# Optimization experiments

Hardware: AMD Instinct MI355X
Metric: run time of the kernel (lower is better)

The kernel has to match this reference:

```python
import jax, jax.numpy as jnp
import numpy as np

N = 50000      # nodes (src = dst at both layers)
E = 800000     # edges per layer
T = 8          # time steps
C_IN = 16      # input channels
HID = 16       # conv1 out channels (hardcoded in SAGENet)
C_OUT = 32     # final out channels


def setup_inputs() -> dict:
    key = jax.random.key(0)
    ks = jax.random.split(key, 10)
    X = jax.random.normal(ks[0], (T, N, C_IN), dtype=jnp.float32)
    edge_index0 = jax.random.randint(ks[1], (2, E), 0, N, dtype=jnp.int32)
    edge_weight0 = jax.random.uniform(ks[2], (E,), dtype=jnp.float32)
    edge_index1 = jax.random.randint(ks[3], (2, E), 0, N, dtype=jnp.int32)
    edge_weight1 = jax.random.uniform(ks[4], (E,), dtype=jnp.float32)
    res_n_id0 = jnp.arange(N, dtype=jnp.int32)
    res_n_id1 = jnp.arange(N, dtype=jnp.int32)
    W1 = jax.random.normal(ks[5], (2 * C_IN, HID), dtype=jnp.float32) * 0.1
    b1 = jax.random.normal(ks[6], (HID,), dtype=jnp.float32) * 0.1
    W2 = jax.random.normal(ks[7], (2 * HID, C_OUT), dtype=jnp.float32) * 0.1
    b2 = jax.random.normal(ks[8], (C_OUT,), dtype=jnp.float32) * 0.1
    return {"X": X, "edge_index0": edge_index0, "edge_weight0": edge_weight0,
            "edge_index1": edge_index1, "edge_weight1": edge_weight1,
            "res_n_id0": res_n_id0, "res_n_id1": res_n_id1,
            "W1": W1, "b1": b1, "W2": W2, "b2": b2}


def sage_conv(x, edge_index, edge_weight, res_n_id, num_dst, W, b):
    # x: [N_src, T, C]; message = edge_weight * x[src]; mean-aggregate to dst;
    # concat residual x[res_n_id] then linear (old PyG SAGEConv, concat=True).
    src, dst = edge_index[0], edge_index[1]
    msg = x[src] * edge_weight[:, None, None]                      # [E, T, C]
    summed = jax.ops.segment_sum(msg, dst, num_segments=num_dst)   # [Nd, T, C]
    cnt = jax.ops.segment_sum(jnp.ones_like(edge_weight), dst, num_segments=num_dst)
    aggr = summed / jnp.maximum(cnt, 1.0)[:, None, None]
    h = jnp.concatenate([x[res_n_id], aggr], axis=-1)              # [Nd, T, 2C]
    return jnp.einsum('ntc,cd->ntd', h, W) + b


def reference(X, edge_index0, edge_weight0, edge_index1, edge_weight1,
              res_n_id0, res_n_id1, W1, b1, W2, b2):
    x = jnp.transpose(X, (1, 0, 2))                                # [N, T, C]
    x = jax.nn.leaky_relu(sage_conv(x, edge_index0, edge_weight0, res_n_id0, N, W1, b1), 0.01)
    x = jax.nn.leaky_relu(sage_conv(x, edge_index1, edge_weight1, res_n_id1, N, W2, b2), 0.01)
    return jnp.transpose(x, (1, 0, 2))                             # [T, N, C_out]
```

## Files before the change

### kernel.cpp

```cpp
#include <hip/hip_runtime.h>
#include <hip/hip_bf16.h>
#include <stdint.h>

static constexpr int Nn   = 50000;
static constexpr int Ee   = 800000;
static constexpr int Tt   = 8;
static constexpr int CIN  = 16;
static constexpr int HID  = 16;
static constexpr int COUT = 32;
static constexpr int TC   = Tt * CIN;
static constexpr int ROWD = TC / 2;

static constexpr int NB  = (2 * Nn + 255) / 256;
static constexpr int CAP = 16;

static constexpr int WBUF_FLOATS = 1584;

__device__ inline float bflo(uint32_t u) { return __uint_as_float(u << 16); }
__device__ inline float bfhi(uint32_t u) { return __uint_as_float(u & 0xffff0000u); }
__device__ inline unsigned short f2bf(float x) {
    __hip_bfloat16 h = __float2bfloat16(x);
    unsigned short u; __builtin_memcpy(&u, &h, 2); return u;
}
__device__ inline uint32_t bfpack(float a, float b) {
    return (uint32_t)f2bf(a) | ((uint32_t)f2bf(b) << 16);
}

__global__ void k_detect_stage(const unsigned short* __restrict__ x16, int nvals,
                               int* __restrict__ flag,
                               const void* W1, const void* b1,
                               const void* W2, const void* b2,
                               float* __restrict__ wbuf,
                               int* __restrict__ bucketCnt) {
    __shared__ int bad;
    if (threadIdx.x == 0) bad = 0;
    __syncthreads();
    for (int i = threadIdx.x; i < nvals; i += 256) {
        int ex = (x16[i] >> 7) & 0xFF;
        if (ex >= 0x8D) atomicOr(&bad, 1);
    }
    __syncthreads();
    int f = bad;
    if (threadIdx.x == 0) flag[0] = f;
    for (int i = threadIdx.x; i < NB; i += 256) bucketCnt[i] = 0;
    for (int i = threadIdx.x; i < WBUF_FLOATS; i += 256) {
        const void* src; int idx;
        if (i < 512)       { src = W1; idx = i; }
        else if (i < 528)  { src = b1; idx = i - 512; }
        else if (i < 1552) { src = W2; idx = i - 528; }
        else               { src = b2; idx = i - 1552; }
        wbuf[i] = f ? ((const float*)src)[idx]
                    : __bfloat162float(((const __hip_bfloat16*)src)[idx]);
    }
}


__global__ __launch_bounds__(256) void k_count(const int* __restrict__ ei0,
                                               const int* __restrict__ ei1,
                                               int* __restrict__ bucketCnt) {
    __shared__ int hist[NB];
    for (int i = threadIdx.x; i < NB; i += 256) hist[i] = 0;
    __syncthreads();
    const int4* d0 = (const int4*)(ei0 + Ee);
    const int4* d1 = (const int4*)(ei1 + Ee);
    int stride = gridDim.x * 256;
    int nq = Ee / 4;
    for (int i = blockIdx.x * 256 + threadIdx.x; i < 2 * nq; i += stride) {
        int4 v; int addn;
        if (i < nq) { v = d0[i]; addn = 0; }
        else        { v = d1[i - nq]; addn = Nn; }
        atomicAdd(&hist[(v.x + addn) >> 8], 1);
        atomicAdd(&hist[(v.y + addn) >> 8], 1);
        atomicAdd(&hist[(v.z + addn) >> 8], 1);
        atomicAdd(&hist[(v.w + addn) >> 8], 1);
    }
    __syncthreads();
    for (int i = threadIdx.x; i < NB; i += 256)
        if (hist[i]) atomicAdd(&bucketCnt[i], hist[i]);
}

__global__ void k_bucketscan(const int* __restrict__ bucketCnt,
                             int* __restrict__ base, int* __restrict__ gcur) {
    __shared__ int tmp[512];
    int tid = threadIdx.x;
    int v = (tid < NB) ? bucketCnt[tid] : 0;
    tmp[tid] = v;
    __syncthreads();
    for (int ofs = 1; ofs < 512; ofs <<= 1) {
        int t = (tid >= ofs) ? tmp[tid - ofs] : 0;
        __syncthreads();
        tmp[tid] += t;
        __syncthreads();
    }
    if (tid < NB) { int b = tmp[tid] - v; base[tid] = b; gcur[tid] = b; }
    if (tid == 0) base[NB] = 2 * Ee;
}

__global__ __launch_bounds__(256) void k_bin(const int* __restrict__ flag,
        const int* __restrict__ ei0, const void* w0v,
        const int* __restrict__ ei1, const void* w1v,
        int* __restrict__ gcur, uint64_t* __restrict__ gout) {
    __shared__ uint64_t rows[NB][CAP];
    __shared__ int cnt[NB];
    int tid = threadIdx.x;
    for (int i = tid; i < NB; i += 256) cnt[i] = 0;
    __syncthreads();
    int f = flag[0];
    int tileStride = gridDim.x * 256;
    for (int base_e = blockIdx.x * 256; base_e < 2 * Ee; base_e += tileStride) {
        int e = base_e + tid;
        if (e < 2 * Ee) {
            int g; uint32_t src, wb;
            if (e < Ee) {
                g = ei0[Ee + e];
                src = (uint32_t)ei0[e];
                wb = f ? f2bf(((const float*)w0v)[e]) : ((const unsigned short*)w0v)[e];
            } else {
                int e1 = e - Ee;
                g = Nn + ei1[Ee + e1];
                src = (uint32_t)ei1[e1];
                wb = f ? f2bf(((const float*)w1v)[e1]) : ((const unsigned short*)w1v)[e1];
            }
            uint64_t r = ((uint64_t)(uint32_t)g << 32) | (src << 16) | wb;
            int b = g >> 8;
            int idx = atomicAdd(&cnt[b], 1);
            if (idx < CAP) rows[b][idx] = r;
            else { int pos = atomicAdd(&gcur[b], 1); gout[pos] = r; }
        }
        __syncthreads();
        for (int b = tid; b < NB; b += 256) {
            if (cnt[b] >= CAP) {
                int pos = atomicAdd(&gcur[b], CAP);
#pragma unroll
                for (int k = 0; k < CAP; k++) gout[pos + k] = rows[b][k];
                cnt[b] = 0;
            }
        }
        __syncthreads();
    }
    for (int b = tid; b < NB; b += 256) {
        int c = cnt[b];
        if (c > 0) {
            int pos = atomicAdd(&gcur[b], c);
            for (int k = 0; k < c; k++) gout[pos + k] = rows[b][k];
        }
    }
}

__global__ __launch_bounds__(256) void k_csr(const int* __restrict__ base,
        const uint64_t* __restrict__ gout,
        int* __restrict__ off, uint32_t* __restrict__ rec) {
    __shared__ int hist[256];
    __shared__ int tmp[256];
    __shared__ int cur[256];
    __shared__ uint32_t stage[8192];
    int b = blockIdx.x, tid = threadIdx.x;
    int lo = base[b], hi = base[b + 1];
    hist[tid] = 0;
    __syncthreads();
    for (int i = lo + tid; i < hi; i += 256) {
        int gl = (int)(gout[i] >> 32) & 255;
        atomicAdd(&hist[gl], 1);
    }
    __syncthreads();
    int v = hist[tid];
    tmp[tid] = v;
    __syncthreads();
    for (int ofs = 1; ofs < 256; ofs <<= 1) {
        int t = (tid >= ofs) ? tmp[tid - ofs] : 0;
        __syncthreads();
        tmp[tid] += t;
        __syncthreads();
    }
    int excl = tmp[tid] - v;
    int gg = (b << 8) + tid;
    if (gg < 2 * Nn) off[gg] = lo + excl;
    if (b == NB - 1 && tid == 0) off[2 * Nn] = 2 * Ee;
    int count = hi - lo;
    if (count <= 8192) {
        cur[tid] = excl;
        __syncthreads();
        for (int i = lo + tid; i < hi; i += 256) {
            uint64_t r = gout[i];
            int gl = (int)(r >> 32) & 255;
            int pos = atomicAdd(&cur[gl], 1);
            stage[pos] = (uint32_t)r;
        }
        __syncthreads();
        for (int i = tid; i < count; i += 256) rec[lo + i] = stage[i];
    } else {
        cur[tid] = lo + excl;
        __syncthreads();
        for (int i = lo + tid; i < hi; i += 256) {
            uint64_t r = gout[i];
            int gl = (int)(r >> 32) & 255;
            int pos = atomicAdd(&cur[gl], 1);
            rec[pos] = (uint32_t)r;
        }
    }
}

__global__ void k_transpose(const int* __restrict__ flag, const void* Xv,
                            uint32_t* __restrict__ xrows) {
    int f = flag[0];
    int i = blockIdx.x * blockDim.x + threadIdx.x;
    if (i >= Nn * ROWD) return;
    int n = i >> 6;
    int l = i & 63;
    int t = l >> 3;
    int c = (l & 7) * 2;
    int sidx = (t * Nn + n) * CIN + c;
    uint32_t v;
    if (f) {
        float2 ab = ((const float2*)Xv)[sidx >> 1];
        v = bfpack(ab.x, ab.y);
    } else {
        const unsigned short* u = (const unsigned short*)Xv;
        v = (uint32_t)u[sidx] | ((uint32_t)u[sidx + 1] << 16);
    }
    xrows[i] = v;
}


__global__ __launch_bounds__(256) void k_layer1(
    const uint32_t* __restrict__ xrows, const int* __restrict__ off,
    const uint32_t* __restrict__ rec, const int* __restrict__ resid,
    const float* __restrict__ wbuf, uint32_t* __restrict__ h1rows) {
    __shared__ float Ws[32 * 16];
    __shared__ float bs[16];
    __shared__ float sh[4][256];
    int tid = threadIdx.x;
    int wv = tid >> 6, lane = tid & 63;
    for (int i = tid; i < 512; i += 256) Ws[i] = wbuf[i];
    if (tid < 16) bs[tid] = wbuf[512 + tid];
    __syncthreads();
    int n = blockIdx.x * 4 + wv;
    int o0 = __builtin_amdgcn_readfirstlane(off[n]);
    int o1 = __builtin_amdgcn_readfirstlane(off[n + 1]);
    int rn = __builtin_amdgcn_readfirstlane(resid[n]);
    uint32_t xv = xrows[rn * ROWD + lane];
    float alo = 0.f, ahi = 0.f;
    int j = o0;
    for (; j + 8 <= o1; j += 8) {
        uint32_t e[8], g[8];
#pragma unroll
        for (int k = 0; k < 8; k++) e[k] = rec[j + k];
#pragma unroll
        for (int k = 0; k < 8; k++) g[k] = xrows[(e[k] >> 16) * ROWD + lane];
#pragma unroll
        for (int k = 0; k < 8; k++) {
            float w = bflo(e[k]);
            alo += w * bflo(g[k]);
            ahi += w * bfhi(g[k]);
        }
    }
    for (; j < o1; j++) {
        uint32_t e0 = rec[j];
        uint32_t g0 = xrows[(e0 >> 16) * ROWD + lane];
        float w0 = bflo(e0);
        alo += w0 * bflo(g0);
        ahi += w0 * bfhi(g0);
    }
    float inv = 1.f / (float)max(o1 - o0, 1);
    float* xs = &sh[wv][0];
    float* ag = &sh[wv][128];
    xs[2 * lane] = bflo(xv);
    xs[2 * lane + 1] = bfhi(xv);
    ag[2 * lane] = alo * inv;
    ag[2 * lane + 1] = ahi * inv;
    int t = lane >> 3;
    int c0 = (2 * lane) & 15;
    const float* xr = &xs[t * 16];
    const float* ar = &ag[t * 16];
    float v0 = bs[c0], v1 = bs[c0 + 1];
#pragma unroll
    for (int k = 0; k < 16; k++) {
        float xk = xr[k], ak = ar[k];
        v0 += xk * Ws[k * 16 + c0] + ak * Ws[(16 + k) * 16 + c0];
        v1 += xk * Ws[k * 16 + c0 + 1] + ak * Ws[(16 + k) * 16 + c0 + 1];
    }
    v0 = v0 > 0.f ? v0 : 0.01f * v0;
    v1 = v1 > 0.f ? v1 : 0.01f * v1;
    h1rows[n * ROWD + lane] = bfpack(v0, v1);
}

__global__ __launch_bounds__(256) void k_layer2(
    const int* __restrict__ flag,
    const uint32_t* __restrict__ h1rows, const int* __restrict__ off,
    const uint32_t* __restrict__ rec, const int* __restrict__ resid,
    const float* __restrict__ wbuf, void* __restrict__ outv) {
    __shared__ float Ws[32 * 32];
    __shared__ float bs[32];
    __shared__ float sh[4][256];
    int tid = threadIdx.x;
    int wv = tid >> 6, lane = tid & 63;
    for (int i = tid; i < 1024; i += 256) Ws[i] = wbuf[528 + i];
    if (tid < 32) bs[tid] = wbuf[1552 + tid];
    __syncthreads();
    int f = flag[0];
    int n = blockIdx.x * 4 + wv;
    int o0 = __builtin_amdgcn_readfirstlane(off[Nn + n]);
    int o1 = __builtin_amdgcn_readfirstlane(off[Nn + n + 1]);
    int rn = __builtin_amdgcn_readfirstlane(resid[n]);
    uint32_t xv = h1rows[rn * ROWD + lane];
    float alo = 0.f, ahi = 0.f;
    int j = o0;
    for (; j + 8 <= o1; j += 8) {
        uint32_t e[8], g[8];
#pragma unroll
        for (int k = 0; k < 8; k++) e[k] = rec[j + k];
#pragma unroll
        for (int k = 0; k < 8; k++) g[k] = h1rows[(e[k] >> 16) * ROWD + lane];
#pragma unroll
        for (int k = 0; k < 8; k++) {
            float w = bflo(e[k]);
            alo += w * bflo(g[k]);
            ahi += w * bfhi(g[k]);
        }
    }
    for (; j < o1; j++) {
        uint32_t e0 = rec[j];
        uint32_t g0 = h1rows[(e0 >> 16) * ROWD + lane];
        float w0 = bflo(e0);
        alo += w0 * bflo(g0);
        ahi += w0 * bfhi(g0);
    }
    float inv = 1.f / (float)max(o1 - o0, 1);
    float* xs = &sh[wv][0];
    float* ag = &sh[wv][128];
    xs[2 * lane] = bflo(xv);
    xs[2 * lane + 1] = bfhi(xv);
    ag[2 * lane] = alo * inv;
    ag[2 * lane + 1] = ahi * inv;
    int h = lane & 31;
    int tb = lane >> 5;
#pragma unroll
    for (int q = 0; q < 4; q++) {
        int t = tb + 2 * q;
        const float* xr = &xs[t * 16];
        const float* ar = &ag[t * 16];
        float v = bs[h];
#pragma unroll
        for (int k = 0; k < 16; k++) {
            v += xr[k] * Ws[k * 32 + h] + ar[k] * Ws[(16 + k) * 32 + h];
        }
        v = v > 0.f ? v : 0.01f * v;
        size_t idx = ((size_t)(t * Nn + n)) * COUT + h;
        if (f) ((float*)outv)[idx] = v;
        else   ((__hip_bfloat16*)outv)[idx] = __float2bfloat16(v);
    }
}


extern "C" void kernel_launch(void* const* d_in, const int* in_sizes, int n_in,
                              void* d_out, int out_size, void* d_ws, size_t ws_size,
                              hipStream_t stream) {
    const void* X   = d_in[0];
    const int* ei0  = (const int*)d_in[1];
    const void* w0  = d_in[2];
    const int* ei1  = (const int*)d_in[3];
    const void* w1  = d_in[4];
    const int* rn0  = (const int*)d_in[5];
    const int* rn1  = (const int*)d_in[6];
    const void* W1  = d_in[7];
    const void* b1  = d_in[8];
    const void* W2  = d_in[9];
    const void* b2  = d_in[10];

    char* ws = (char*)d_ws;
    size_t p = 0;
    auto alloc = [&](size_t bytes) -> char* {
        p = (p + 255) & ~(size_t)255;
        char* r = ws + p;
        p += bytes;
        return r;
    };
    int* flag       = (int*)alloc(4);
    float* wbuf     = (float*)alloc(WBUF_FLOATS * 4);
    int* bucketCnt  = (int*)alloc(NB * 4);
    int* base       = (int*)alloc((NB + 1) * 4);
    int* gcur       = (int*)alloc(NB * 4);
    int* off        = (int*)alloc(((size_t)2 * Nn + 1) * 4);
    uint32_t* recf  = (uint32_t*)alloc((size_t)2 * Ee * 4);
    uint32_t* h1rows= (uint32_t*)alloc((size_t)Nn * ROWD * 4);
    uint64_t* gout  = (uint64_t*)alloc((size_t)2 * Ee * 8);
    uint32_t* xrows = (uint32_t*)gout;

    hipLaunchKernelGGL(k_detect_stage, dim3(1), dim3(256), 0, stream,
                       (const unsigned short*)X, 16384, flag, W1, b1, W2, b2,
                       wbuf, bucketCnt);
    hipLaunchKernelGGL(k_count, dim3(256), dim3(256), 0, stream,
                       ei0, ei1, bucketCnt);
    hipLaunchKernelGGL(k_bucketscan, dim3(1), dim3(512), 0, stream,
                       bucketCnt, base, gcur);
    hipLaunchKernelGGL(k_bin, dim3(512), dim3(256), 0, stream,
                       flag, ei0, w0, ei1, w1, gcur, gout);
    hipLaunchKernelGGL(k_csr, dim3(NB), dim3(256), 0, stream,
                       base, gout, off, recf);
    hipLaunchKernelGGL(k_transpose, dim3((Nn * ROWD + 255) / 256), dim3(256), 0, stream,
                       flag, X, xrows);
    hipLaunchKernelGGL(k_layer1, dim3(Nn / 4), dim3(256), 0, stream,
                       xrows, off, recf, rn0, wbuf, h1rows);
    hipLaunchKernelGGL(k_layer2, dim3(Nn / 4), dim3(256), 0, stream,
                       flag, h1rows, off, recf, rn1, wbuf, d_out);
    (void)in_sizes; (void)n_in; (void)out_size; (void)ws_size;
}
```

Baseline: 276.3 us.

## Use MFMA for SAGE linear layers and 16-byte gathers with edge-parallel lanes

Both layer kernels now gather neighbor rows as 16-byte uint4 loads, with four lane groups each handling a different edge and a cross-lane shuffle reduction at the end. This replaces the per-lane 4-byte loads over edges. The dense concat-then-linear step now runs as bf16 MFMA 16x16x32 instructions on weights pre-packed by the setup kernel, instead of scalar FMAs reading float weights from shared memory. The binning kernel also processes four edges per thread per tile. The cost is that the aggregate and weights are rounded to bf16 before the matmul, which may change accuracy in fp32 mode.

```diff
diff --git a/kernel.cpp b/kernel.cpp
--- a/kernel.cpp
+++ b/kernel.cpp
@@ -14,7 +14,9 @@
 static constexpr int NB  = (2 * Nn + 255) / 256;
 static constexpr int CAP = 16;
 
-static constexpr int WBUF_FLOATS = 1584;
+typedef __attribute__((ext_vector_type(8))) short short8;
+typedef __attribute__((ext_vector_type(4))) float f32x4;
+union FU { uint4 u4; short8 s8; };
 
 __device__ inline float bflo(uint32_t u) { return __uint_as_float(u << 16); }
 __device__ inline float bfhi(uint32_t u) { return __uint_as_float(u & 0xffff0000u); }
@@ -25,33 +27,50 @@
 __device__ inline uint32_t bfpack(float a, float b) {
     return (uint32_t)f2bf(a) | ((uint32_t)f2bf(b) << 16);
 }
+__device__ inline void fma8(float2& a0, float2& a1, float2& a2, float2& a3,
+                            float w, uint4 r) {
+    a0.x += w * bflo(r.x); a0.y += w * bfhi(r.x);
+    a1.x += w * bflo(r.y); a1.y += w * bfhi(r.y);
+    a2.x += w * bflo(r.z); a2.y += w * bfhi(r.z);
+    a3.x += w * bflo(r.w); a3.y += w * bfhi(r.w);
+}
+__device__ inline void redg(float2& a) {
+    a.x += __shfl_xor(a.x, 16); a.y += __shfl_xor(a.y, 16);
+    a.x += __shfl_xor(a.x, 32); a.y += __shfl_xor(a.y, 32);
+}
 
 __global__ void k_detect_stage(const unsigned short* __restrict__ x16, int nvals,
                                int* __restrict__ flag,
                                const void* W1, const void* b1,
                                const void* W2, const void* b2,
-                               float* __restrict__ wbuf,
+                               float* __restrict__ biasbuf,
+                               uint32_t* __restrict__ wpk1,
+                               uint32_t* __restrict__ wpk2,
                                int* __restrict__ bucketCnt) {
     __shared__ int bad;
-    if (threadIdx.x == 0) bad = 0;
-    __syncthreads();
-    for (int i = threadIdx.x; i < nvals; i += 256) {
+    int tid = threadIdx.x;
+    if (tid == 0) bad = 0;
+    __syncthreads();
+    for (int i = tid; i < nvals; i += 256) {
         int ex = (x16[i] >> 7) & 0xFF;
         if (ex >= 0x8D) atomicOr(&bad, 1);
     }
     __syncthreads();
     int f = bad;
-    if (threadIdx.x == 0) flag[0] = f;
-    for (int i = threadIdx.x; i < NB; i += 256) bucketCnt[i] = 0;
-    for (int i = threadIdx.x; i < WBUF_FLOATS; i += 256) {
-        const void* src; int idx;
-        if (i < 512)       { src = W1; idx = i; }
-        else if (i < 528)  { src = b1; idx = i - 512; }
-        else if (i < 1552) { src = W2; idx = i - 528; }
-        else               { src = b2; idx = i - 1552; }
-        wbuf[i] = f ? ((const float*)src)[idx]
-                    : __bfloat162float(((const __hip_bfloat16*)src)[idx]);
-    }
+    if (tid == 0) flag[0] = f;
+    auto ldf = [&](const void* srcp, int idx) -> float {
+        return f ? ((const float*)srcp)[idx]
+                 : __bfloat162float(((const __hip_bfloat16*)srcp)[idx]);
+    };
+    if (tid < 16) biasbuf[tid] = ldf(b1, tid);
+    if (tid >= 16 && tid < 48) biasbuf[tid] = ldf(b2, tid - 16);
+    { int h = tid >> 4, d = tid & 15;
+      wpk1[tid] = bfpack(ldf(W1, 2 * d * 16 + h), ldf(W1, (2 * d + 1) * 16 + h)); }
+    for (int i = tid; i < 512; i += 256) {
+        int h = i >> 4, d = i & 15;
+        wpk2[i] = bfpack(ldf(W2, 2 * d * 32 + h), ldf(W2, (2 * d + 1) * 32 + h));
+    }
+    for (int i = tid; i < NB; i += 256) bucketCnt[i] = 0;
 }
 
 
@@ -106,26 +125,31 @@
     for (int i = tid; i < NB; i += 256) cnt[i] = 0;
     __syncthreads();
     int f = flag[0];
-    int tileStride = gridDim.x * 256;
-    for (int base_e = blockIdx.x * 256; base_e < 2 * Ee; base_e += tileStride) {
-        int e = base_e + tid;
-        if (e < 2 * Ee) {
-            int g; uint32_t src, wb;
-            if (e < Ee) {
-                g = ei0[Ee + e];
-                src = (uint32_t)ei0[e];
-                wb = f ? f2bf(((const float*)w0v)[e]) : ((const unsigned short*)w0v)[e];
-            } else {
-                int e1 = e - Ee;
-                g = Nn + ei1[Ee + e1];
-                src = (uint32_t)ei1[e1];
-                wb = f ? f2bf(((const float*)w1v)[e1]) : ((const unsigned short*)w1v)[e1];
+    int tileStride = gridDim.x * 1024;
+    for (int base_e = blockIdx.x * 1024; base_e < 2 * Ee; base_e += tileStride) {
+#pragma unroll
+        for (int s = 0; s < 4; s++) {
+            int e = base_e + s * 256 + tid;
+            if (e < 2 * Ee) {
+                int g; uint32_t src, wb;
+                if (e < Ee) {
+                    g = ei0[Ee + e];
+                    src = (uint32_t)ei0[e];
+                    wb = f ? f2bf(((const float*)w0v)[e])
+                           : ((const unsigned short*)w0v)[e];
+                } else {
+                    int e1 = e - Ee;
+                    g = Nn + ei1[Ee + e1];
+                    src = (uint32_t)ei1[e1];
+                    wb = f ? f2bf(((const float*)w1v)[e1])
+                           : ((const unsigned short*)w1v)[e1];
+                }
+                uint64_t r = ((uint64_t)(uint32_t)g << 32) | (src << 16) | wb;
+                int b = g >> 8;
+                int idx = atomicAdd(&cnt[b], 1);
+                if (idx < CAP) rows[b][idx] = r;
+                else { int pos = atomicAdd(&gcur[b], 1); gout[pos] = r; }
             }
-            uint64_t r = ((uint64_t)(uint32_t)g << 32) | (src << 16) | wb;
-            int b = g >> 8;
-            int idx = atomicAdd(&cnt[b], 1);
-            if (idx < CAP) rows[b][idx] = r;
-            else { int pos = atomicAdd(&gcur[b], 1); gout[pos] = r; }
         }
         __syncthreads();
         for (int b = tid; b < NB; b += 256) {
@@ -225,129 +249,126 @@
 __global__ __launch_bounds__(256) void k_layer1(
     const uint32_t* __restrict__ xrows, const int* __restrict__ off,
     const uint32_t* __restrict__ rec, const int* __restrict__ resid,
-    const float* __restrict__ wbuf, uint32_t* __restrict__ h1rows) {
-    __shared__ float Ws[32 * 16];
-    __shared__ float bs[16];
-    __shared__ float sh[4][256];
-    int tid = threadIdx.x;
-    int wv = tid >> 6, lane = tid & 63;
-    for (int i = tid; i < 512; i += 256) Ws[i] = wbuf[i];
-    if (tid < 16) bs[tid] = wbuf[512 + tid];
-    __syncthreads();
+    const uint32_t* __restrict__ wpk1, const float* __restrict__ biasbuf,
+    uint32_t* __restrict__ h1rows) {
+    __shared__ __align__(16) uint32_t shA[32 * 20];
+    int tid = threadIdx.x, wv = tid >> 6, lane = tid & 63;
+    int g = lane >> 4, p = lane & 15;
+    uint4 bfr = ((const uint4*)wpk1)[p * 4 + g];
+    float bias = biasbuf[p];
     int n = blockIdx.x * 4 + wv;
     int o0 = __builtin_amdgcn_readfirstlane(off[n]);
     int o1 = __builtin_amdgcn_readfirstlane(off[n + 1]);
     int rn = __builtin_amdgcn_readfirstlane(resid[n]);
-    uint32_t xv = xrows[rn * ROWD + lane];
-    float alo = 0.f, ahi = 0.f;
-    int j = o0;
-    for (; j + 8 <= o1; j += 8) {
-        uint32_t e[8], g[8];
+    const uint4* xb = (const uint4*)xrows;
+    uint4 xs4 = xb[rn * 16 + p];
+    float2 a0 = {0.f, 0.f}, a1 = a0, a2 = a0, a3 = a0;
+    for (int j = o0; j < o1; j += 8) {
+        int j0 = j + g, j1 = j + 4 + g;
+        uint32_t e0 = rec[min(j0, o1 - 1)];
+        uint32_t e1 = rec[min(j1, o1 - 1)];
+        uint4 r0 = xb[(int)(e0 >> 16) * 16 + p];
+        uint4 r1 = xb[(int)(e1 >> 16) * 16 + p];
+        float w0 = (j0 < o1) ? bflo(e0) : 0.f;
+        float w1 = (j1 < o1) ? bflo(e1) : 0.f;
+        fma8(a0, a1, a2, a3, w0, r0);
+        fma8(a0, a1, a2, a3, w1, r1);
+    }
+    redg(a0); redg(a1); redg(a2); redg(a3);
+    float inv = 1.f / (float)max(o1 - o0, 1);
+    uint4 agp;
+    agp.x = bfpack(a0.x * inv, a0.y * inv);
+    agp.y = bfpack(a1.x * inv, a1.y * inv);
+    agp.z = bfpack(a2.x * inv, a2.y * inv);
+    agp.w = bfpack(a3.x * inv, a3.y * inv);
+    int r = wv * 8 + (p >> 1);
+    int hs = (p & 1) * 4;
+    if (g == 0)      *(uint4*)&shA[r * 20 + hs] = xs4;
+    else if (g == 1) *(uint4*)&shA[r * 20 + 8 + hs] = agp;
+    __syncthreads();
+    FU fa, fb; fb.u4 = bfr;
+    fa.u4 = *(const uint4*)&shA[((wv >> 1) * 16 + p) * 20 + 4 * g];
+    f32x4 acc = {bias, bias, bias, bias};
+    acc = __builtin_amdgcn_mfma_f32_16x16x32_bf16(fa.s8, fb.s8, acc, 0, 0, 0);
+    bool mine = ((g >> 1) == (wv & 1));
 #pragma unroll
-        for (int k = 0; k < 8; k++) e[k] = rec[j + k];
-#pragma unroll
-        for (int k = 0; k < 8; k++) g[k] = xrows[(e[k] >> 16) * ROWD + lane];
-#pragma unroll
-        for (int k = 0; k < 8; k++) {
-            float w = bflo(e[k]);
-            alo += w * bflo(g[k]);
-            ahi += w * bfhi(g[k]);
-        }
-    }
-    for (; j < o1; j++) {
-        uint32_t e0 = rec[j];
-        uint32_t g0 = xrows[(e0 >> 16) * ROWD + lane];
-        float w0 = bflo(e0);
-        alo += w0 * bflo(g0);
-        ahi += w0 * bfhi(g0);
-    }
-    float inv = 1.f / (float)max(o1 - o0, 1);
-    float* xs = &sh[wv][0];
-    float* ag = &sh[wv][128];
-    xs[2 * lane] = bflo(xv);
-    xs[2 * lane + 1] = bfhi(xv);
-    ag[2 * lane] = alo * inv;
-    ag[2 * lane + 1] = ahi * inv;
-    int t = lane >> 3;
-    int c0 = (2 * lane) & 15;
-    const float* xr = &xs[t * 16];
-    const float* ar = &ag[t * 16];
-    float v0 = bs[c0], v1 = bs[c0 + 1];
-#pragma unroll
-    for (int k = 0; k < 16; k++) {
-        float xk = xr[k], ak = ar[k];
-        v0 += xk * Ws[k * 16 + c0] + ak * Ws[(16 + k) * 16 + c0];
-        v1 += xk * Ws[k * 16 + c0 + 1] + ak * Ws[(16 + k) * 16 + c0 + 1];
-    }
-    v0 = v0 > 0.f ? v0 : 0.01f * v0;
-    v1 = v1 > 0.f ? v1 : 0.01f * v1;
-    h1rows[n * ROWD + lane] = bfpack(v0, v1);
+    for (int rg = 0; rg < 4; rg++) {
+        float v = acc[rg];
+        v = fmaxf(v, 0.01f * v);
+        float vn = __shfl_xor(v, 1);
+        if (mine && !(p & 1)) {
+            int t = (g & 1) * 4 + rg;
+            h1rows[n * 64 + t * 8 + (p >> 1)] = bfpack(v, vn);
+        }
+    }
 }
 
 __global__ __launch_bounds__(256) void k_layer2(
     const int* __restrict__ flag,
     const uint32_t* __restrict__ h1rows, const int* __restrict__ off,
     const uint32_t* __restrict__ rec, const int* __restrict__ resid,
-    const float* __restrict__ wbuf, void* __restrict__ outv) {
-    __shared__ float Ws[32 * 32];
-    __shared__ float bs[32];
-    __shared__ float sh[4][256];
-    int tid = threadIdx.x;
-    int wv = tid >> 6, lane = tid & 63;
-    for (int i = tid; i < 1024; i += 256) Ws[i] = wbuf[528 + i];
-    if (tid < 32) bs[tid] = wbuf[1552 + tid];
-    __syncthreads();
+    const uint32_t* __restrict__ wpk2, const float* __restrict__ biasbuf,
+    void* __restrict__ outv) {
+    __shared__ __align__(16) uint32_t shA[32 * 20];
+    int tid = threadIdx.x, wv = tid >> 6, lane = tid & 63;
+    int g = lane >> 4, p = lane & 15;
+    uint4 b0 = ((const uint4*)wpk2)[p * 4 + g];
+    uint4 b1v = ((const uint4*)wpk2)[(p + 16) * 4 + g];
+    float bias0 = biasbuf[16 + p];
+    float bias1 = biasbuf[32 + p];
     int f = flag[0];
     int n = blockIdx.x * 4 + wv;
     int o0 = __builtin_amdgcn_readfirstlane(off[Nn + n]);
     int o1 = __builtin_amdgcn_readfirstlane(off[Nn + n + 1]);
     int rn = __builtin_amdgcn_readfirstlane(resid[n]);
-    uint32_t xv = h1rows[rn * ROWD + lane];
-    float alo = 0.f, ahi = 0.f;
-    int j = o0;
-    for (; j + 8 <= o1; j += 8) {
-        uint32_t e[8], g[8];
+    const uint4* xb = (const uint4*)h1rows;
+    uint4 xs4 = xb[rn * 16 + p];
+    float2 a0 = {0.f, 0.f}, a1 = a0, a2 = a0, a3 = a0;
+    for (int j = o0; j < o1; j += 8) {
+        int j0 = j + g, j1 = j + 4 + g;
+        uint32_t e0 = rec[min(j0, o1 - 1)];
+        uint32_t e1 = rec[min(j1, o1 - 1)];
+        uint4 r0 = xb[(int)(e0 >> 16) * 16 + p];
+        uint4 r1 = xb[(int)(e1 >> 16) * 16 + p];
+        float w0 = (j0 < o1) ? bflo(e0) : 0.f;
+        float w1 = (j1 < o1) ? bflo(e1) : 0.f;
+        fma8(a0, a1, a2, a3, w0, r0);
+        fma8(a0, a1, a2, a3, w1, r1);
+    }
+    redg(a0); redg(a1); redg(a2); redg(a3);
+    float inv = 1.f / (float)max(o1 - o0, 1);
+    uint4 agp;
+    agp.x = bfpack(a0.x * inv, a0.y * inv);
+    agp.y = bfpack(a1.x * inv, a1.y * inv);
+    agp.z = bfpack(a2.x * inv, a2.y * inv);
+    agp.w = bfpack(a3.x * inv, a3.y * inv);
+    int r = wv * 8 + (p >> 1);
+    int hs = (p & 1) * 4;
+    if (g == 0)      *(uint4*)&shA[r * 20 + hs] = xs4;
+    else if (g == 1) *(uint4*)&shA[r * 20 + 8 + hs] = agp;
+    __syncthreads();
+    FU fa, fb0, fb1; fb0.u4 = b0; fb1.u4 = b1v;
+    fa.u4 = *(const uint4*)&shA[((wv >> 1) * 16 + p) * 20 + 4 * g];
+    f32x4 acc0 = {bias0, bias0, bias0, bias0};
+    f32x4 acc1 = {bias1, bias1, bias1, bias1};
+    acc0 = __builtin_amdgcn_mfma_f32_16x16x32_bf16(fa.s8, fb0.s8, acc0, 0, 0, 0);
+    acc1 = __builtin_amdgcn_mfma_f32_16x16x32_bf16(fa.s8, fb1.s8, acc1, 0, 0, 0);
+    bool mine = ((g >> 1) == (wv & 1));
+    if (mine) {
 #pragma unroll
-        for (int k = 0; k < 8; k++) e[k] = rec[j + k];
-#pragma unroll
-        for (int k = 0; k < 8; k++) g[k] = h1rows[(e[k] >> 16) * ROWD + lane];
-#pragma unroll
-        for (int k = 0; k < 8; k++) {
-            float w = bflo(e[k]);
-            alo += w * bflo(g[k]);
-            ahi += w * bfhi(g[k]);
-        }
-    }
-    for (; j < o1; j++) {
-        uint32_t e0 = rec[j];
-        uint32_t g0 = h1rows[(e0 >> 16) * ROWD + lane];
-        float w0 = bflo(e0);
-        alo += w0 * bflo(g0);
-        ahi += w0 * bfhi(g0);
-    }
-    float inv = 1.f / (float)max(o1 - o0, 1);
-    float* xs = &sh[wv][0];
-    float* ag = &sh[wv][128];
-    xs[2 * lane] = bflo(xv);
-    xs[2 * lane + 1] = bfhi(xv);
-    ag[2 * lane] = alo * inv;
-    ag[2 * lane + 1] = ahi * inv;
-    int h = lane & 31;
-    int tb = lane >> 5;
-#pragma unroll
-    for (int q = 0; q < 4; q++) {
-        int t = tb + 2 * q;
-        const float* xr = &xs[t * 16];
-        const float* ar = &ag[t * 16];
-        float v = bs[h];
-#pragma unroll
-        for (int k = 0; k < 16; k++) {
-            v += xr[k] * Ws[k * 32 + h] + ar[k] * Ws[(16 + k) * 32 + h];
-        }
-        v = v > 0.f ? v : 0.01f * v;
-        size_t idx = ((size_t)(t * Nn + n)) * COUT + h;
-        if (f) ((float*)outv)[idx] = v;
-        else   ((__hip_bfloat16*)outv)[idx] = __float2bfloat16(v);
+        for (int rg = 0; rg < 4; rg++) {
+            int t = (g & 1) * 4 + rg;
+            size_t idx = ((size_t)(t * Nn + n)) * COUT + p;
+            float v = acc0[rg]; v = fmaxf(v, 0.01f * v);
+            float u = acc1[rg]; u = fmaxf(u, 0.01f * u);
+            if (f) {
+                ((float*)outv)[idx] = v;
+                ((float*)outv)[idx + 16] = u;
+            } else {
+                ((__hip_bfloat16*)outv)[idx] = __float2bfloat16(v);
+                ((__hip_bfloat16*)outv)[idx + 16] = __float2bfloat16(u);
+            }
+        }
     }
 }
 
@@ -375,20 +396,22 @@
         p += bytes;
         return r;
     };
-    int* flag       = (int*)alloc(4);
-    float* wbuf     = (float*)alloc(WBUF_FLOATS * 4);
-    int* bucketCnt  = (int*)alloc(NB * 4);
-    int* base       = (int*)alloc((NB + 1) * 4);
-    int* gcur       = (int*)alloc(NB * 4);
-    int* off        = (int*)alloc(((size_t)2 * Nn + 1) * 4);
-    uint32_t* recf  = (uint32_t*)alloc((size_t)2 * Ee * 4);
-    uint32_t* h1rows= (uint32_t*)alloc((size_t)Nn * ROWD * 4);
-    uint64_t* gout  = (uint64_t*)alloc((size_t)2 * Ee * 8);
-    uint32_t* xrows = (uint32_t*)gout;
+    int* flag        = (int*)alloc(4);
+    float* biasbuf   = (float*)alloc(48 * 4);
+    uint32_t* wpk1   = (uint32_t*)alloc(256 * 4);
+    uint32_t* wpk2   = (uint32_t*)alloc(512 * 4);
+    int* bucketCnt   = (int*)alloc(NB * 4);
+    int* base        = (int*)alloc((NB + 1) * 4);
+    int* gcur        = (int*)alloc(NB * 4);
+    int* off         = (int*)alloc(((size_t)2 * Nn + 1) * 4);
+    uint32_t* recf   = (uint32_t*)alloc((size_t)2 * Ee * 4);
+    uint32_t* h1rows = (uint32_t*)alloc((size_t)Nn * ROWD * 4);
+    uint64_t* gout   = (uint64_t*)alloc((size_t)2 * Ee * 8);
+    uint32_t* xrows  = (uint32_t*)gout;
 
     hipLaunchKernelGGL(k_detect_stage, dim3(1), dim3(256), 0, stream,
                        (const unsigned short*)X, 16384, flag, W1, b1, W2, b2,
-                       wbuf, bucketCnt);
+                       biasbuf, wpk1, wpk2, bucketCnt);
     hipLaunchKernelGGL(k_count, dim3(256), dim3(256), 0, stream,
                        ei0, ei1, bucketCnt);
     hipLaunchKernelGGL(k_bucketscan, dim3(1), dim3(512), 0, stream,
@@ -400,8 +423,8 @@
     hipLaunchKernelGGL(k_transpose, dim3((Nn * ROWD + 255) / 256), dim3(256), 0, stream,
                        flag, X, xrows);
     hipLaunchKernelGGL(k_layer1, dim3(Nn / 4), dim3(256), 0, stream,
-                       xrows, off, recf, rn0, wbuf, h1rows);
+                       xrows, off, recf, rn0, wpk1, biasbuf, h1rows);
     hipLaunchKernelGGL(k_layer2, dim3(Nn / 4), dim3(256), 0, stream,
-                       flag, h1rows, off, recf, rn1, wbuf, d_out);
+                       flag, h1rows, off, recf, rn1, wpk2, biasbuf, d_out);
     (void)in_sizes; (void)n_in; (void)out_size; (void)ws_size;
 }
```

After: 268.6 us. -2.8%, faster.
